# Optimization experiments

Hardware: AMD Instinct MI355X
Metric: run time of the kernel (lower is better)

The kernel has to match this reference:

```python
import jax, jax.numpy as jnp
import numpy as np

NUM_HEADS = 4  # nn.MultiheadAttention(num_heads=4)


def setup_inputs() -> dict:
    key = jax.random.key(0)
    ks = jax.random.split(key, 9)
    E, D, B, S = 16, 128, 8, 512
    H2 = D // 2
    s = 0.05
    return {
        "lstm_features": jax.random.normal(ks[0], (B, S, D), dtype=jnp.float32),
        "Wqkv": jax.random.normal(ks[1], (E, 3 * D, D), dtype=jnp.float32) * s,
        "bqkv": jax.random.normal(ks[2], (E, 3 * D), dtype=jnp.float32) * s,
        "Wo": jax.random.normal(ks[3], (E, D, D), dtype=jnp.float32) * s,
        "bo": jax.random.normal(ks[4], (E, D), dtype=jnp.float32) * s,
        "W1": jax.random.normal(ks[5], (E, H2, D), dtype=jnp.float32) * s,
        "b1": jax.random.normal(ks[6], (E, H2), dtype=jnp.float32) * s,
        "W2": jax.random.normal(ks[7], (E, 1, H2), dtype=jnp.float32) * s,
        "b2": jax.random.normal(ks[8], (E, 1), dtype=jnp.float32) * s,
    }


def reference(lstm_features, Wqkv, bqkv, Wo, bo, W1, b1, W2, b2):
    # lstm_features: [B, S, D]; params stacked over E=num_events.
    B, S, D = lstm_features.shape
    E = Wqkv.shape[0]
    H = NUM_HEADS
    Dh = D // H

    # Grouped in-projection for all events at once: [E, B, S, 3D]
    qkv = jnp.einsum("bsd,ekd->ebsk", lstm_features, Wqkv) + bqkv[:, None, None, :]
    q, k, v = jnp.split(qkv, 3, axis=-1)  # each [E, B, S, D]

    def heads(t):  # [E,B,S,D] -> [E,B,H,S,Dh]
        return t.reshape(E, B, S, H, Dh).transpose(0, 1, 3, 2, 4)

    q, k, v = heads(q), heads(k), heads(v)

    scale = 1.0 / jnp.sqrt(jnp.asarray(Dh, dtype=lstm_features.dtype))
    scores = jnp.einsum("ebhqd,ebhkd->ebhqk", q, k) * scale  # [E,B,H,S,S]
    attn = jax.nn.softmax(scores, axis=-1)
    ctx = jnp.einsum("ebhqk,ebhkd->ebhqd", attn, v)  # [E,B,H,S,Dh]
    ctx = ctx.transpose(0, 1, 3, 2, 4).reshape(E, B, S, D)

    attended = jnp.einsum("ebsd,eod->ebso", ctx, Wo) + bo[:, None, None, :]

    # Per-event MLP head: D -> D//2 -> 1 (dropout is identity in eval)
    h = jax.nn.relu(jnp.einsum("ebsd,ehd->ebsh", attended, W1) + b1[:, None, None, :])
    logits = jnp.einsum("ebsh,eoh->ebso", h, W2) + b2[:, None, None, :]  # [E,B,S,1]
    logits = logits[..., 0]  # [E,B,S]

    # torch.stack(..., dim=2) -> [B, S, E]
    return logits.transpose(1, 2, 0)
```

## Files before the change

kernel.cpp:

```cpp
#include <hip/hip_runtime.h>
#include <hip/hip_bf16.h>


#define E_ 16
#define B_ 8
#define S_ 512
#define D_ 128
#define H_ 4
#define DH_ 32
#define H2_ 64
#define M_ (B_ * S_)
#define QK_SCALE_L2E 0.25503472437616588f

#define ATTN_LDS_BYTES (512 * 80 + 32 * 1040)
#define HEAD_LDS_BYTES (128 * 136 * 2 * 2)
#define QKV_LDS_BYTES  (128 * 136 * 2 * 2)

typedef __attribute__((ext_vector_type(4))) short bf16x4;
typedef __attribute__((ext_vector_type(8))) short bf16x8;
typedef __attribute__((ext_vector_type(4))) float f32x4;

__device__ __forceinline__ short f2bf(float f) {
    unsigned u = __builtin_bit_cast(unsigned, f);
    u += 0x7fffu + ((u >> 16) & 1u);
    return (short)(u >> 16);
}

__device__ __forceinline__ unsigned pk2(float lo, float hi) {
    __hip_bfloat162 t = __float22bfloat162_rn(make_float2(lo, hi));
    unsigned r;
    __builtin_memcpy(&r, &t, sizeof(r));
    return r;
}

__device__ __forceinline__ bf16x8 cat8(bf16x4 lo, bf16x4 hi) {
    return __builtin_shufflevector(lo, hi, 0, 1, 2, 3, 4, 5, 6, 7);
}

__global__ __launch_bounds__(256) void convert_kernel(
    const float* __restrict__ x, const float* __restrict__ w,
    const float* __restrict__ wo, const float* __restrict__ w1,
    short* __restrict__ xbf, short* __restrict__ wbf,
    short* __restrict__ wobf, short* __restrict__ w1bf)
{
    const int XN  = (M_ * D_) / 8;
    const int WN  = (E_ * 3 * D_ * D_) / 8;
    const int WON = (E_ * D_ * D_) / 8;
    const int W1N = (E_ * H2_ * D_) / 8;
    int idx = blockIdx.x * 256 + threadIdx.x;
    const float* src; short* dst; int off;
    if (idx < XN)                        { src = x;  dst = xbf;  off = idx; }
    else if (idx < XN + WN)              { src = w;  dst = wbf;  off = idx - XN; }
    else if (idx < XN + WN + WON)        { src = wo; dst = wobf; off = idx - XN - WN; }
    else if (idx < XN + WN + WON + W1N)  { src = w1; dst = w1bf; off = idx - XN - WN - WON; }
    else return;
    float4 v0 = *(const float4*)&src[(size_t)off * 8];
    float4 v1 = *(const float4*)&src[(size_t)off * 8 + 4];
    bf16x8 o;
    o[0] = f2bf(v0.x); o[1] = f2bf(v0.y); o[2] = f2bf(v0.z); o[3] = f2bf(v0.w);
    o[4] = f2bf(v1.x); o[5] = f2bf(v1.y); o[6] = f2bf(v1.z); o[7] = f2bf(v1.w);
    *(bf16x8*)&dst[(size_t)off * 8] = o;
}

__global__ __launch_bounds__(512) void qkv_mfma_kernel(
    const short* __restrict__ xbf,
    const short* __restrict__ wbf,
    const float* __restrict__ bqkv,
    short* __restrict__ q, short* __restrict__ k, short* __restrict__ v)
{
    extern __shared__ __align__(16) char lds[];
    short (*xs)[136] = (short(*)[136])lds;
    short (*ws)[136] = (short(*)[136])(lds + 128 * 136 * 2);

    const int ct2 = blockIdx.x;
    const int rt  = blockIdx.y;
    const int e   = blockIdx.z;
    const int tid = threadIdx.x;
    const int w    = tid >> 6;
    const int lane = tid & 63;
    const int l15  = lane & 15;
    const int g    = lane >> 4;

    #pragma unroll
    for (int p = 0; p < 4; ++p) {
        int idx = tid + p * 512;
        int row = idx >> 4, c8 = (idx & 15) * 8;
        *(bf16x8*)&xs[row][c8] =
            *(const bf16x8*)&xbf[(size_t)(rt * 128 + row) * 128 + c8];
        *(bf16x8*)&ws[row][c8] =
            *(const bf16x8*)&wbf[((size_t)e * 384 + ct2 * 128 + row) * 128 + c8];
    }
    __syncthreads();

    const int m0 = (w >> 2) * 64;
    const int n0 = (w & 3) * 32;
    f32x4 acc[4][2] = {};

    #pragma unroll
    for (int kk = 0; kk < 128; kk += 32) {
        bf16x8 A0 = cat8(*(const bf16x4*)&ws[n0      + l15][kk + 4 * g],
                         *(const bf16x4*)&ws[n0      + l15][kk + 16 + 4 * g]);
        bf16x8 A1 = cat8(*(const bf16x4*)&ws[n0 + 16 + l15][kk + 4 * g],
                         *(const bf16x4*)&ws[n0 + 16 + l15][kk + 16 + 4 * g]);
        #pragma unroll
        for (int mm = 0; mm < 4; ++mm) {
            bf16x8 Bm = cat8(*(const bf16x4*)&xs[m0 + mm * 16 + l15][kk + 4 * g],
                             *(const bf16x4*)&xs[m0 + mm * 16 + l15][kk + 16 + 4 * g]);
            acc[mm][0] = __builtin_amdgcn_mfma_f32_16x16x32_bf16(A0, Bm, acc[mm][0], 0, 0, 0);
            acc[mm][1] = __builtin_amdgcn_mfma_f32_16x16x32_bf16(A1, Bm, acc[mm][1], 0, 0, 0);
        }
    }

    if (ct2 < 2) {
        short* dst = (ct2 == 0) ? q : k;
        const float scale = (ct2 == 0) ? QK_SCALE_L2E : 1.0f;
        #pragma unroll
        for (int mm = 0; mm < 4; ++mm) {
            #pragma unroll
            for (int nn = 0; nn < 2; ++nn) {
                const int d  = n0 + nn * 16 + 4 * g;
                const int h  = d >> 5, dh = d & 31;
                const int jb = ct2 * 128 + d;
                const float b0 = bqkv[e * 384 + jb + 0];
                const float b1 = bqkv[e * 384 + jb + 1];
                const float b2 = bqkv[e * 384 + jb + 2];
                const float b3 = bqkv[e * 384 + jb + 3];
                const int m  = rt * 128 + m0 + mm * 16 + l15;
                const int bb = m >> 9, s = m & 511;
                bf16x4 o;
                o[0] = f2bf((acc[mm][nn][0] + b0) * scale);
                o[1] = f2bf((acc[mm][nn][1] + b1) * scale);
                o[2] = f2bf((acc[mm][nn][2] + b2) * scale);
                o[3] = f2bf((acc[mm][nn][3] + b3) * scale);
                *(bf16x4*)&dst[((((size_t)e * B_ + bb) * H_ + h) * S_ + s) * DH_ + dh] = o;
            }
        }
    } else {
        __syncthreads();
        float (*rp)[132] = (float(*)[132])lds;
        #pragma unroll
        for (int mm = 0; mm < 4; ++mm) {
            #pragma unroll
            for (int nn = 0; nn < 2; ++nn) {
                const int jl = n0 + nn * 16 + 4 * g;
                const int ml = m0 + mm * 16 + l15;
                rp[jl + 0][ml] = acc[mm][nn][0];
                rp[jl + 1][ml] = acc[mm][nn][1];
                rp[jl + 2][ml] = acc[mm][nn][2];
                rp[jl + 3][ml] = acc[mm][nn][3];
            }
        }
        __syncthreads();
        const int bb = (rt * 128) >> 9;
        const int sb = (rt * 128) & 511;
        #pragma unroll
        for (int p = 0; p < 4; ++p) {
            int task = tid + p * 512;
            int jl = task >> 4, sc = (task & 15) * 8;
            const int h = jl >> 5, dh = jl & 31;
            const float bias = bqkv[e * 384 + 256 + jl];
            bf16x8 o;
            #pragma unroll
            for (int j = 0; j < 8; ++j) o[j] = f2bf(rp[jl][sc + j] + bias);
            *(bf16x8*)&v[((((size_t)e * B_ + bb) * H_ + h) * DH_ + dh) * S_ + sb + sc] = o;
        }
    }
}

__global__ __launch_bounds__(512) void attn_kernel(
    const short* __restrict__ q, const short* __restrict__ k,
    const short* __restrict__ vt, short* __restrict__ ctxbf)
{
    extern __shared__ __align__(16) char smem[];
    char* Kbase  = smem;
    char* VTbase = smem + 40960;

    const int bh  = blockIdx.x;
    const int e   = blockIdx.y;
    const int tid = threadIdx.x;
    const int w    = tid >> 6;
    const int lane = tid & 63;
    const int l15  = lane & 15;
    const int g    = lane >> 4;

    const size_t base = ((size_t)e * 32 + bh) * (S_ * DH_);
    const short* qg = q  + base;
    const short* kg = k  + base;
    const short* vg = vt + base;

    {
        const uint4* src = (const uint4*)(kg + (size_t)tid * DH_);
        uint4* dst = (uint4*)(Kbase + (size_t)tid * 80);
        dst[0] = src[0]; dst[1] = src[1]; dst[2] = src[2]; dst[3] = src[3];
    }
    {
        int d = tid >> 4, c0 = (tid & 15) * 32;
        const uint4* src = (const uint4*)(vg + (size_t)d * S_ + c0);
        uint4* dst = (uint4*)(VTbase + (size_t)d * 1040 + c0 * 2);
        dst[0] = src[0]; dst[1] = src[1]; dst[2] = src[2]; dst[3] = src[3];
    }
    bf16x8 bq[4];
    #pragma unroll
    for (int qf = 0; qf < 4; ++qf) {
        const short* qp = qg + (size_t)(w * 64 + qf * 16 + l15) * DH_;
        bq[qf] = cat8(*(const bf16x4*)(qp + 4 * g),
                      *(const bf16x4*)(qp + 16 + 4 * g));
    }
    __syncthreads();

    f32x4 acc0[4] = {}, acc1[4] = {};
    float lsum[4] = {0.f, 0.f, 0.f, 0.f};

    for (int kt = 0; kt < 16; ++kt) {
        bf16x8 ka[2];
        #pragma unroll
        for (int tt = 0; tt < 2; ++tt) {
            const int row_l = (kt * 2 + tt) * 16 + l15;
            const char* kp = Kbase + (size_t)row_l * 80 + g * 8;
            ka[tt] = cat8(*(const bf16x4*)kp, *(const bf16x4*)(kp + 32));
        }
        const int keyb = kt * 32;
        const char* vp = VTbase + (size_t)l15 * 1040 + (keyb + 4 * g) * 2;
        bf16x8 va0 = cat8(*(const bf16x4*)vp, *(const bf16x4*)(vp + 32));
        const char* vp1 = vp + 16 * 1040;
        bf16x8 va1 = cat8(*(const bf16x4*)vp1, *(const bf16x4*)(vp1 + 32));

        #pragma unroll
        for (int qf = 0; qf < 4; ++qf) {
            f32x4 z = {0.f, 0.f, 0.f, 0.f};
            f32x4 s0 = __builtin_amdgcn_mfma_f32_16x16x32_bf16(ka[0], bq[qf], z, 0, 0, 0);
            f32x4 s1 = __builtin_amdgcn_mfma_f32_16x16x32_bf16(ka[1], bq[qf], z, 0, 0, 0);
            float p0 = __builtin_amdgcn_exp2f(s0[0]);
            float p1 = __builtin_amdgcn_exp2f(s0[1]);
            float p2 = __builtin_amdgcn_exp2f(s0[2]);
            float p3 = __builtin_amdgcn_exp2f(s0[3]);
            float p4 = __builtin_amdgcn_exp2f(s1[0]);
            float p5 = __builtin_amdgcn_exp2f(s1[1]);
            float p6 = __builtin_amdgcn_exp2f(s1[2]);
            float p7 = __builtin_amdgcn_exp2f(s1[3]);
            lsum[qf] += ((p0 + p1) + (p2 + p3)) + ((p4 + p5) + (p6 + p7));
            uint4 uu = make_uint4(pk2(p0, p1), pk2(p2, p3),
                                  pk2(p4, p5), pk2(p6, p7));
            bf16x8 pf = __builtin_bit_cast(bf16x8, uu);
            acc0[qf] = __builtin_amdgcn_mfma_f32_16x16x32_bf16(va0, pf, acc0[qf], 0, 0, 0);
            acc1[qf] = __builtin_amdgcn_mfma_f32_16x16x32_bf16(va1, pf, acc1[qf], 0, 0, 0);
        }
    }

    const int b = bh >> 2, h = bh & 3;
    #pragma unroll
    for (int qf = 0; qf < 4; ++qf) {
        float ls = lsum[qf];
        ls += __shfl_xor(ls, 16);
        ls += __shfl_xor(ls, 32);
        const float inv = 1.0f / ls;
        const int qrow = w * 64 + qf * 16 + l15;
        short* cg = ctxbf + (((size_t)(e * B_ + b) * S_ + qrow) * D_ + h * DH_);
        bf16x4 o0, o1;
        #pragma unroll
        for (int r = 0; r < 4; ++r) {
            o0[r] = f2bf(acc0[qf][r] * inv);
            o1[r] = f2bf(acc1[qf][r] * inv);
        }
        *(bf16x4*)&cg[4 * g]      = o0;
        *(bf16x4*)&cg[16 + 4 * g] = o1;
    }
}

__global__ __launch_bounds__(512) void head_mfma_kernel(
    const short* __restrict__ ctxbf,
    const short* __restrict__ wobf,
    const float* __restrict__ bo,
    const short* __restrict__ w1bf,
    const float* __restrict__ b1,
    const float* __restrict__ W2,
    const float* __restrict__ b2,
    float* __restrict__ out)
{
    extern __shared__ __align__(16) char smem[];
    short (*Wos)[136] = (short(*)[136])smem;
    short (*cts)[136] = (short(*)[136])(smem + 128 * 136 * 2);

    const int mt  = blockIdx.x;
    const int e   = blockIdx.y;
    const int tid = threadIdx.x;
    const int w    = tid >> 6;
    const int lane = tid & 63;
    const int l15  = lane & 15;
    const int g    = lane >> 4;

    #pragma unroll
    for (int p = 0; p < 4; ++p) {
        int idx = tid + p * 512;
        int row = idx >> 4, c8 = (idx & 15) * 8;
        *(bf16x8*)&Wos[row][c8] =
            *(const bf16x8*)&wobf[((size_t)e * 128 + row) * 128 + c8];
        *(bf16x8*)&cts[row][c8] =
            *(const bf16x8*)&ctxbf[((size_t)e * M_ + mt * 128 + row) * 128 + c8];
    }
    __syncthreads();

    f32x4 accA[8] = {};
    #pragma unroll
    for (int kk = 0; kk < 128; kk += 32) {
        bf16x8 a = cat8(*(const bf16x4*)&cts[w * 16 + l15][kk + 4 * g],
                        *(const bf16x4*)&cts[w * 16 + l15][kk + 16 + 4 * g]);
        #pragma unroll
        for (int t = 0; t < 8; ++t) {
            bf16x8 bfr = cat8(*(const bf16x4*)&Wos[t * 16 + l15][kk + 4 * g],
                              *(const bf16x4*)&Wos[t * 16 + l15][kk + 16 + 4 * g]);
            accA[t] = __builtin_amdgcn_mfma_f32_16x16x32_bf16(a, bfr, accA[t], 0, 0, 0);
        }
    }
    __syncthreads();

    #pragma unroll
    for (int p = 0; p < 2; ++p) {
        int idx = tid + p * 512;
        int row = idx >> 4, c8 = (idx & 15) * 8;
        *(bf16x8*)&Wos[row][c8] =
            *(const bf16x8*)&w1bf[((size_t)e * 64 + row) * 128 + c8];
    }
    #pragma unroll
    for (int t = 0; t < 8; ++t) {
        const float bov = bo[e * 128 + t * 16 + l15];
        #pragma unroll
        for (int r = 0; r < 4; ++r)
            cts[w * 16 + 4 * g + r][t * 16 + l15] = f2bf(accA[t][r] + bov);
    }
    __syncthreads();

    f32x4 accB[4] = {};
    #pragma unroll
    for (int kk = 0; kk < 128; kk += 32) {
        bf16x8 a = cat8(*(const bf16x4*)&cts[w * 16 + l15][kk + 4 * g],
                        *(const bf16x4*)&cts[w * 16 + l15][kk + 16 + 4 * g]);
        #pragma unroll
        for (int t = 0; t < 4; ++t) {
            bf16x8 bfr = cat8(*(const bf16x4*)&Wos[t * 16 + l15][kk + 4 * g],
                              *(const bf16x4*)&Wos[t * 16 + l15][kk + 16 + 4 * g]);
            accB[t] = __builtin_amdgcn_mfma_f32_16x16x32_bf16(a, bfr, accB[t], 0, 0, 0);
        }
    }

    float b1v[4], w2v[4];
    #pragma unroll
    for (int t = 0; t < 4; ++t) {
        b1v[t] = b1[e * 64 + t * 16 + l15];
        w2v[t] = W2[e * 64 + t * 16 + l15];
    }
    const float b2v = b2[e];
    #pragma unroll
    for (int r = 0; r < 4; ++r) {
        float s = 0.f;
        #pragma unroll
        for (int t = 0; t < 4; ++t)
            s += fmaxf(accB[t][r] + b1v[t], 0.f) * w2v[t];
        s += __shfl_xor(s, 1);
        s += __shfl_xor(s, 2);
        s += __shfl_xor(s, 4);
        s += __shfl_xor(s, 8);
        if (l15 == 0) {
            const int m = mt * 128 + w * 16 + 4 * g + r;
            const int bb = m >> 9, ss = m & 511;
            out[((size_t)(bb * S_ + ss)) * E_ + e] = s + b2v;
        }
    }
}

extern "C" void kernel_launch(void* const* d_in, const int* in_sizes, int n_in,
                              void* d_out, int out_size, void* d_ws, size_t ws_size,
                              hipStream_t stream) {
    const float* x    = (const float*)d_in[0];
    const float* Wqkv = (const float*)d_in[1];
    const float* bqkv = (const float*)d_in[2];
    const float* Wo   = (const float*)d_in[3];
    const float* bo   = (const float*)d_in[4];
    const float* W1   = (const float*)d_in[5];
    const float* b1   = (const float*)d_in[6];
    const float* W2   = (const float*)d_in[7];
    const float* b2   = (const float*)d_in[8];
    float* out = (float*)d_out;

    const size_t SZ = (size_t)E_ * B_ * H_ * S_ * DH_;
    short* qb    = (short*)d_ws;
    short* kb    = qb + SZ;
    short* vtb   = kb + SZ;
    short* ctxbf = vtb + SZ;
    short* xbf   = ctxbf + SZ;
    short* wbf   = xbf + (size_t)M_ * D_;
    short* wobf  = wbf + (size_t)E_ * 3 * D_ * D_;
    short* w1bf  = wobf + (size_t)E_ * D_ * D_;

    hipFuncSetAttribute((const void*)qkv_mfma_kernel,
                        hipFuncAttributeMaxDynamicSharedMemorySize,
                        QKV_LDS_BYTES);
    hipFuncSetAttribute((const void*)attn_kernel,
                        hipFuncAttributeMaxDynamicSharedMemorySize,
                        ATTN_LDS_BYTES);
    hipFuncSetAttribute((const void*)head_mfma_kernel,
                        hipFuncAttributeMaxDynamicSharedMemorySize,
                        HEAD_LDS_BYTES);

    convert_kernel<<<dim3(832), 256, 0, stream>>>(x, Wqkv, Wo, W1, xbf, wbf, wobf, w1bf);
    qkv_mfma_kernel<<<dim3(3, 32, 16), 512, QKV_LDS_BYTES, stream>>>(xbf, wbf, bqkv, qb, kb, vtb);
    attn_kernel<<<dim3(32, 16), 512, ATTN_LDS_BYTES, stream>>>(qb, kb, vtb, ctxbf);
    head_mfma_kernel<<<dim3(32, 16), 512, HEAD_LDS_BYTES, stream>>>(ctxbf, wobf, bo, w1bf, b1, W2, b2, out);
}
```

Before: 74.71 us.

## Split attention queries across two blocks and stream K tiles through smaller LDS

```diff
diff --git a/kernel.cpp b/kernel.cpp
--- a/kernel.cpp
+++ b/kernel.cpp
@@ -12,7 +12,6 @@
 #define M_ (B_ * S_)
 #define QK_SCALE_L2E 0.25503472437616588f
 
-#define ATTN_LDS_BYTES (512 * 80 + 32 * 1040)
 #define HEAD_LDS_BYTES (128 * 136 * 2 * 2)
 #define QKV_LDS_BYTES  (128 * 136 * 2 * 2)
 
@@ -171,12 +170,12 @@
     const short* __restrict__ q, const short* __restrict__ k,
     const short* __restrict__ vt, short* __restrict__ ctxbf)
 {
-    extern __shared__ __align__(16) char smem[];
-    char* Kbase  = smem;
-    char* VTbase = smem + 40960;
-
-    const int bh  = blockIdx.x;
-    const int e   = blockIdx.y;
+    __shared__ alignas(16) short Ks[128][40];
+    __shared__ alignas(16) short VTs[32][520];
+
+    const int qh  = blockIdx.x;
+    const int bh  = blockIdx.y;
+    const int e   = blockIdx.z;
     const int tid = threadIdx.x;
     const int w    = tid >> 6;
     const int lane = tid & 63;
@@ -189,78 +188,125 @@
     const short* vg = vt + base;
 
     {
-        const uint4* src = (const uint4*)(kg + (size_t)tid * DH_);
-        uint4* dst = (uint4*)(Kbase + (size_t)tid * 80);
-        dst[0] = src[0]; dst[1] = src[1]; dst[2] = src[2]; dst[3] = src[3];
-    }
-    {
         int d = tid >> 4, c0 = (tid & 15) * 32;
         const uint4* src = (const uint4*)(vg + (size_t)d * S_ + c0);
-        uint4* dst = (uint4*)(VTbase + (size_t)d * 1040 + c0 * 2);
+        uint4* dst = (uint4*)((char*)&VTs[0][0] + (size_t)d * 1040 + c0 * 2);
         dst[0] = src[0]; dst[1] = src[1]; dst[2] = src[2]; dst[3] = src[3];
     }
-    bf16x8 bq[4];
-    #pragma unroll
-    for (int qf = 0; qf < 4; ++qf) {
-        const short* qp = qg + (size_t)(w * 64 + qf * 16 + l15) * DH_;
-        bq[qf] = cat8(*(const bf16x4*)(qp + 4 * g),
-                      *(const bf16x4*)(qp + 16 + 4 * g));
+    {
+        int row = tid >> 2, ch = (tid & 3) * 8;
+        *(uint4*)((char*)&Ks[0][0] + (size_t)row * 80 + ch * 2) =
+            *(const uint4*)(kg + (size_t)row * DH_ + ch);
+    }
+    bf16x8 bq0, bq1;
+    {
+        const short* qp = qg + (size_t)(qh * 256 + w * 32 + l15) * DH_;
+        bq0 = cat8(*(const bf16x4*)(qp + 4 * g), *(const bf16x4*)(qp + 16 + 4 * g));
+        qp += 16 * DH_;
+        bq1 = cat8(*(const bf16x4*)(qp + 4 * g), *(const bf16x4*)(qp + 16 + 4 * g));
     }
     __syncthreads();
 
-    f32x4 acc0[4] = {}, acc1[4] = {};
-    float lsum[4] = {0.f, 0.f, 0.f, 0.f};
-
-    for (int kt = 0; kt < 16; ++kt) {
-        bf16x8 ka[2];
-        #pragma unroll
-        for (int tt = 0; tt < 2; ++tt) {
-            const int row_l = (kt * 2 + tt) * 16 + l15;
-            const char* kp = Kbase + (size_t)row_l * 80 + g * 8;
-            ka[tt] = cat8(*(const bf16x4*)kp, *(const bf16x4*)(kp + 32));
-        }
-        const int keyb = kt * 32;
-        const char* vp = VTbase + (size_t)l15 * 1040 + (keyb + 4 * g) * 2;
-        bf16x8 va0 = cat8(*(const bf16x4*)vp, *(const bf16x4*)(vp + 32));
-        const char* vp1 = vp + 16 * 1040;
-        bf16x8 va1 = cat8(*(const bf16x4*)vp1, *(const bf16x4*)(vp1 + 32));
-
-        #pragma unroll
-        for (int qf = 0; qf < 4; ++qf) {
-            f32x4 z = {0.f, 0.f, 0.f, 0.f};
-            f32x4 s0 = __builtin_amdgcn_mfma_f32_16x16x32_bf16(ka[0], bq[qf], z, 0, 0, 0);
-            f32x4 s1 = __builtin_amdgcn_mfma_f32_16x16x32_bf16(ka[1], bq[qf], z, 0, 0, 0);
-            float p0 = __builtin_amdgcn_exp2f(s0[0]);
-            float p1 = __builtin_amdgcn_exp2f(s0[1]);
-            float p2 = __builtin_amdgcn_exp2f(s0[2]);
-            float p3 = __builtin_amdgcn_exp2f(s0[3]);
-            float p4 = __builtin_amdgcn_exp2f(s1[0]);
-            float p5 = __builtin_amdgcn_exp2f(s1[1]);
-            float p6 = __builtin_amdgcn_exp2f(s1[2]);
-            float p7 = __builtin_amdgcn_exp2f(s1[3]);
-            lsum[qf] += ((p0 + p1) + (p2 + p3)) + ((p4 + p5) + (p6 + p7));
-            uint4 uu = make_uint4(pk2(p0, p1), pk2(p2, p3),
-                                  pk2(p4, p5), pk2(p6, p7));
-            bf16x8 pf = __builtin_bit_cast(bf16x8, uu);
-            acc0[qf] = __builtin_amdgcn_mfma_f32_16x16x32_bf16(va0, pf, acc0[qf], 0, 0, 0);
-            acc1[qf] = __builtin_amdgcn_mfma_f32_16x16x32_bf16(va1, pf, acc1[qf], 0, 0, 0);
-        }
-    }
-
-    const int b = bh >> 2, h = bh & 3;
-    #pragma unroll
-    for (int qf = 0; qf < 4; ++qf) {
-        float ls = lsum[qf];
+    f32x4 acc00 = {0.f,0.f,0.f,0.f}, acc01 = {0.f,0.f,0.f,0.f};
+    f32x4 acc10 = {0.f,0.f,0.f,0.f}, acc11 = {0.f,0.f,0.f,0.f};
+    float lsum0 = 0.f, lsum1 = 0.f;
+
+    for (int quarter = 0; quarter < 4; ++quarter) {
+        #pragma unroll 1
+        for (int kt = 0; kt < 4; ++kt) {
+            const char* kp0 = (const char*)&Ks[0][0] + (size_t)(kt * 32 + l15) * 80 + g * 8;
+            bf16x8 ka0 = cat8(*(const bf16x4*)kp0, *(const bf16x4*)(kp0 + 32));
+            const char* kp1 = kp0 + 16 * 80;
+            bf16x8 ka1 = cat8(*(const bf16x4*)kp1, *(const bf16x4*)(kp1 + 32));
+
+            bf16x8 pf0, pf1;
+            {
+                f32x4 z = {0.f, 0.f, 0.f, 0.f};
+                f32x4 s0 = __builtin_amdgcn_mfma_f32_16x16x32_bf16(ka0, bq0, z, 0, 0, 0);
+                f32x4 s1 = __builtin_amdgcn_mfma_f32_16x16x32_bf16(ka1, bq0, z, 0, 0, 0);
+                float p0 = __builtin_amdgcn_exp2f(s0[0]);
+                float p1 = __builtin_amdgcn_exp2f(s0[1]);
+                float p2 = __builtin_amdgcn_exp2f(s0[2]);
+                float p3 = __builtin_amdgcn_exp2f(s0[3]);
+                lsum0 += (p0 + p1) + (p2 + p3);
+                unsigned u0 = pk2(p0, p1), u1 = pk2(p2, p3);
+                p0 = __builtin_amdgcn_exp2f(s1[0]);
+                p1 = __builtin_amdgcn_exp2f(s1[1]);
+                p2 = __builtin_amdgcn_exp2f(s1[2]);
+                p3 = __builtin_amdgcn_exp2f(s1[3]);
+                lsum0 += (p0 + p1) + (p2 + p3);
+                uint4 uu = make_uint4(u0, u1, pk2(p0, p1), pk2(p2, p3));
+                pf0 = __builtin_bit_cast(bf16x8, uu);
+            }
+            {
+                f32x4 z = {0.f, 0.f, 0.f, 0.f};
+                f32x4 s0 = __builtin_amdgcn_mfma_f32_16x16x32_bf16(ka0, bq1, z, 0, 0, 0);
+                f32x4 s1 = __builtin_amdgcn_mfma_f32_16x16x32_bf16(ka1, bq1, z, 0, 0, 0);
+                float p0 = __builtin_amdgcn_exp2f(s0[0]);
+                float p1 = __builtin_amdgcn_exp2f(s0[1]);
+                float p2 = __builtin_amdgcn_exp2f(s0[2]);
+                float p3 = __builtin_amdgcn_exp2f(s0[3]);
+                lsum1 += (p0 + p1) + (p2 + p3);
+                unsigned u0 = pk2(p0, p1), u1 = pk2(p2, p3);
+                p0 = __builtin_amdgcn_exp2f(s1[0]);
+                p1 = __builtin_amdgcn_exp2f(s1[1]);
+                p2 = __builtin_amdgcn_exp2f(s1[2]);
+                p3 = __builtin_amdgcn_exp2f(s1[3]);
+                lsum1 += (p0 + p1) + (p2 + p3);
+                uint4 uu = make_uint4(u0, u1, pk2(p0, p1), pk2(p2, p3));
+                pf1 = __builtin_bit_cast(bf16x8, uu);
+            }
+            const int keyb = quarter * 128 + kt * 32;
+            const char* vp = (const char*)&VTs[0][0] + (size_t)l15 * 1040 + (keyb + 4 * g) * 2;
+            {
+                bf16x8 va = cat8(*(const bf16x4*)vp, *(const bf16x4*)(vp + 32));
+                acc00 = __builtin_amdgcn_mfma_f32_16x16x32_bf16(va, pf0, acc00, 0, 0, 0);
+                acc01 = __builtin_amdgcn_mfma_f32_16x16x32_bf16(va, pf1, acc01, 0, 0, 0);
+            }
+            {
+                const char* vq = vp + 16 * 1040;
+                bf16x8 va = cat8(*(const bf16x4*)vq, *(const bf16x4*)(vq + 32));
+                acc10 = __builtin_amdgcn_mfma_f32_16x16x32_bf16(va, pf0, acc10, 0, 0, 0);
+                acc11 = __builtin_amdgcn_mfma_f32_16x16x32_bf16(va, pf1, acc11, 0, 0, 0);
+            }
+        }
+        if (quarter < 3) {
+            __syncthreads();
+            int row = tid >> 2, ch = (tid & 3) * 8;
+            *(uint4*)((char*)&Ks[0][0] + (size_t)row * 80 + ch * 2) =
+                *(const uint4*)(kg + (size_t)((quarter + 1) * 128 + row) * DH_ + ch);
+            __syncthreads();
+        }
+    }
+
+    {
+        float ls = lsum0;
         ls += __shfl_xor(ls, 16);
         ls += __shfl_xor(ls, 32);
         const float inv = 1.0f / ls;
-        const int qrow = w * 64 + qf * 16 + l15;
-        short* cg = ctxbf + (((size_t)(e * B_ + b) * S_ + qrow) * D_ + h * DH_);
+        short* cg = ctxbf + (((size_t)(e * B_ + (bh >> 2)) * S_ + (qh * 256 + w * 32 + l15)) * D_
+                             + (bh & 3) * DH_);
         bf16x4 o0, o1;
         #pragma unroll
         for (int r = 0; r < 4; ++r) {
-            o0[r] = f2bf(acc0[qf][r] * inv);
-            o1[r] = f2bf(acc1[qf][r] * inv);
+            o0[r] = f2bf(acc00[r] * inv);
+            o1[r] = f2bf(acc10[r] * inv);
+        }
+        *(bf16x4*)&cg[4 * g]      = o0;
+        *(bf16x4*)&cg[16 + 4 * g] = o1;
+    }
+    {
+        float ls = lsum1;
+        ls += __shfl_xor(ls, 16);
+        ls += __shfl_xor(ls, 32);
+        const float inv = 1.0f / ls;
+        short* cg = ctxbf + (((size_t)(e * B_ + (bh >> 2)) * S_ + (qh * 256 + w * 32 + 16 + l15)) * D_
+                             + (bh & 3) * DH_);
+        bf16x4 o0, o1;
+        #pragma unroll
+        for (int r = 0; r < 4; ++r) {
+            o0[r] = f2bf(acc01[r] * inv);
+            o1[r] = f2bf(acc11[r] * inv);
         }
         *(bf16x4*)&cg[4 * g]      = o0;
         *(bf16x4*)&cg[16 + 4 * g] = o1;
@@ -395,15 +441,12 @@
     hipFuncSetAttribute((const void*)qkv_mfma_kernel,
                         hipFuncAttributeMaxDynamicSharedMemorySize,
                         QKV_LDS_BYTES);
-    hipFuncSetAttribute((const void*)attn_kernel,
-                        hipFuncAttributeMaxDynamicSharedMemorySize,
-                        ATTN_LDS_BYTES);
     hipFuncSetAttribute((const void*)head_mfma_kernel,
                         hipFuncAttributeMaxDynamicSharedMemorySize,
                         HEAD_LDS_BYTES);
 
     convert_kernel<<<dim3(832), 256, 0, stream>>>(x, Wqkv, Wo, W1, xbf, wbf, wobf, w1bf);
     qkv_mfma_kernel<<<dim3(3, 32, 16), 512, QKV_LDS_BYTES, stream>>>(xbf, wbf, bqkv, qb, kb, vtb);
-    attn_kernel<<<dim3(32, 16), 512, ATTN_LDS_BYTES, stream>>>(qb, kb, vtb, ctxbf);
+    attn_kernel<<<dim3(2, 32, 16), 512, 0, stream>>>(qb, kb, vtb, ctxbf);
     head_mfma_kernel<<<dim3(32, 16), 512, HEAD_LDS_BYTES, stream>>>(ctxbf, wobf, bo, w1bf, b1, W2, b2, out);
 }
```

Measured after the change: 74.41 us. About the same (-0.4%).
